# Kernel optimization log

Measured on AMD Instinct MI355X. Metric: run time of the kernel, lower is better.

The kernel has to match this reference:

```python
import jax, jax.numpy as jnp
import numpy as np

B, T, H, N = 4, 2048, 1024, 16
DT_MIN, DT_MAX = 1e-3, 1e-1
A_INIT_MIN, A_INIT_MAX = 0.5, 2.0


def _inv_softplus(x):
    # log(exp(x) - 1), numerically stable
    return x + jnp.log(-jnp.expm1(-x))


def setup_inputs() -> dict:
    key = jax.random.key(0)
    kx, ka, kb, kc, kw, kdt = jax.random.split(key, 6)
    x = jax.random.normal(kx, (B, T, H), dtype=jnp.float32)
    A_log = jax.random.uniform(ka, (H, N), minval=np.log(A_INIT_MIN), maxval=np.log(A_INIT_MAX), dtype=jnp.float32)
    B_mat = 0.02 * jax.random.normal(kb, (H, N), dtype=jnp.float32)
    C_mat = 0.02 * jax.random.normal(kc, (H, N), dtype=jnp.float32)
    D_vec = jnp.ones((H,), dtype=jnp.float32)
    W_dt = 0.02 * jax.random.normal(kw, (H, H), dtype=jnp.float32)
    b_dt = _inv_softplus(jax.random.uniform(kdt, (H,), minval=DT_MIN, maxval=DT_MAX, dtype=jnp.float32))
    return {"x": x, "A_log": A_log, "B_mat": B_mat, "C_mat": C_mat, "D_vec": D_vec, "W_dt": W_dt, "b_dt": b_dt}


def reference(x, A_log, B_mat, C_mat, D_vec, W_dt, b_dt):
    # in_proj is Identity since input_size == hidden_size
    u = x  # (B, T, H)
    A = -jnp.exp(A_log)  # (H, N)
    # dt for all timesteps at once: softplus(u @ W_dt^T + b_dt) -> (B, T, H)
    dt = jax.nn.softplus(jnp.einsum('bth,gh->btg', u, W_dt) + b_dt)
    state0 = jnp.zeros((u.shape[0], A_log.shape[0], A_log.shape[1]), dtype=u.dtype)

    def step(state, inp):
        dt_t, u_t = inp  # (B, H), (B, H)
        dtA = dt_t[..., None]  # (B, H, 1)
        A_bar = jnp.exp(dtA * A)                       # (B, H, N)
        state = A_bar * state + (dtA * B_mat) * u_t[..., None]
        y_t = jnp.einsum('bhn,hn->bh', state, C_mat) + D_vec * u_t
        return state, y_t

    # scan over time axis
    state_final, ys = jax.lax.scan(step, state0, (dt.transpose(1, 0, 2), u.transpose(1, 0, 2)))
    out = ys.transpose(1, 0, 2)  # (B, T, H)
    return out, state_final
```

## Files before the change

kernel.cpp:

```cpp
#include <hip/hip_runtime.h>
#include <stdint.h>

#define BB 4
#define TT 2048
#define HH 1024
#define NN 16
#define KK 1024
#define GG 1024
#define MM (BB*TT)
#define NCHUNK 64
#define TC (TT/NCHUNK)
#define HB 256

#if __has_builtin(__builtin_amdgcn_exp2f)
#define FAST_EXP2(x) __builtin_amdgcn_exp2f(x)
#else
#define FAST_EXP2(x) __expf((x) * 0.6931471805599453f)
#endif
#define EXPSCALE 1.4426950408889634f

typedef __attribute__((ext_vector_type(8))) short short8;
typedef __attribute__((ext_vector_type(4))) float f32x4;
typedef __attribute__((ext_vector_type(8))) _Float16 half8;
typedef __attribute__((ext_vector_type(4))) _Float16 half4;

__device__ __forceinline__ unsigned short f2bf(float f) {
  union { float f; unsigned u; } a; a.f = f;
  unsigned u = a.u;
  u += 0x7fffu + ((u >> 16) & 1u);
  return (unsigned short)(u >> 16);
}

__global__ __launch_bounds__(256) void cvt2_f32_bf16(const float* __restrict__ srcA,
                                                     unsigned short* __restrict__ dstA, int n4a,
                                                     const float* __restrict__ srcB,
                                                     unsigned short* __restrict__ dstB, int n4b) {
  int i = blockIdx.x * blockDim.x + threadIdx.x;
  const float* s; unsigned short* d; int j;
  if (i < n4a) { s = srcA; d = dstA; j = i; }
  else         { s = srcB; d = dstB; j = i - n4a; if (j >= n4b) return; }
  float4 a = ((const float4*)s)[j];
  ushort4 o;
  o.x = f2bf(a.x); o.y = f2bf(a.y); o.z = f2bf(a.z); o.w = f2bf(a.w);
  ((ushort4*)d)[j] = o;
}

__global__ __launch_bounds__(256) void gemm_dt(const unsigned short* __restrict__ xb,
                                               const unsigned short* __restrict__ wb,
                                               const float* __restrict__ b_dt,
                                               _Float16* __restrict__ dtH) {
  __shared__ short lsA[128 * 32];
  __shared__ short lsB[64 * 32];
  const int tid  = threadIdx.x;
  const int w    = tid >> 6;
  const int lane = tid & 63;
  const int m0 = blockIdx.x * 128;
  const int g0 = blockIdx.y * 64;

  const int ea  = w * 1024 + lane * 8;
  const int am0 = ea >> 5,         ak0 = ea & 31;
  const int am1 = (ea + 512) >> 5, ak1 = (ea + 512) & 31;
  const int eb  = w * 512 + lane * 8;
  const int bg0 = eb >> 5,         bk0 = eb & 31;
  const unsigned short* gA0 = xb + (size_t)(m0 + am0) * KK + ak0;
  const unsigned short* gA1 = xb + (size_t)(m0 + am1) * KK + ak1;
  const unsigned short* gB0 = wb + (size_t)(g0 + bg0) * KK + bk0;
  short* lA0 = lsA + w * 1024;
  short* lB0 = lsB + w * 512;

  const int wm   = (w >> 1) * 64;
  const int wg   = (w & 1) * 32;
  const int lrow = lane & 15;
  const int lq   = lane >> 4;

  f32x4 acc[4][2];
  const f32x4 zero = {0.f, 0.f, 0.f, 0.f};
#pragma unroll
  for (int i = 0; i < 4; ++i)
#pragma unroll
    for (int j = 0; j < 2; ++j) acc[i][j] = zero;

  for (int kt = 0; kt < KK / 32; ++kt) {
    const int ko = kt * 32;
    __builtin_amdgcn_global_load_lds((__attribute__((address_space(1))) void*)(gA0 + ko),
                                     (__attribute__((address_space(3))) void*)(lA0), 16, 0, 0);
    __builtin_amdgcn_global_load_lds((__attribute__((address_space(1))) void*)(gA1 + ko),
                                     (__attribute__((address_space(3))) void*)(lA0 + 512), 16, 0, 0);
    __builtin_amdgcn_global_load_lds((__attribute__((address_space(1))) void*)(gB0 + ko),
                                     (__attribute__((address_space(3))) void*)(lB0), 16, 0, 0);
    __syncthreads();

    short8 af[4], bfr[2];
#pragma unroll
    for (int mi = 0; mi < 4; ++mi)
      af[mi] = *(const short8*)&lsA[(wm + mi * 16 + lrow) * 32 + lq * 8];
#pragma unroll
    for (int ni = 0; ni < 2; ++ni)
      bfr[ni] = *(const short8*)&lsB[(wg + ni * 16 + lrow) * 32 + lq * 8];
#pragma unroll
    for (int mi = 0; mi < 4; ++mi)
#pragma unroll
      for (int ni = 0; ni < 2; ++ni)
        acc[mi][ni] = __builtin_amdgcn_mfma_f32_16x16x32_bf16(af[mi], bfr[ni], acc[mi][ni], 0, 0, 0);
    __syncthreads();
  }

  const int b  = m0 >> 11;
  const int tb = (m0 & (TT - 1)) + wm + lq * 4;
#pragma unroll
  for (int mi = 0; mi < 4; ++mi)
#pragma unroll
    for (int ni = 0; ni < 2; ++ni) {
      const int gcol = g0 + wg + ni * 16 + lrow;
      const float bias = b_dt[gcol];
      half4 sp;
#pragma unroll
      for (int r = 0; r < 4; ++r) {
        float z = acc[mi][ni][r] + bias;
        sp[r] = (_Float16)(fmaxf(z, 0.f) + __logf(1.f + __expf(-fabsf(z))));
      }
      *(half4*)&dtH[((size_t)b * HH + gcol) * TT + tb + mi * 16] = sp;
    }
}

__global__ __launch_bounds__(256, 4) void ssm_phase1(const float* __restrict__ x,
                                                     const _Float16* __restrict__ dtH,
                                                     const float* __restrict__ A_log,
                                                     float* __restrict__ sloc,
                                                     float* __restrict__ sdArr) {
  __shared__ float uT[TC][HB];
  const int tid = threadIdx.x;
  const int bid = blockIdx.x;
  const int hb = bid & (HH / HB - 1);
  const int b  = (bid >> 2) & (BB - 1);
  const int c  = bid >> 4;
  const int h  = hb * HB + tid;
  const int w    = tid >> 6;
  const int lane = tid & 63;

  const float* xg = x + (size_t)b * TT * HH + (size_t)c * TC * HH + hb * HB;
#pragma unroll
  for (int i = 0; i < 8; ++i) {
    const int t = i * 4 + w;
    __builtin_amdgcn_global_load_lds(
        (__attribute__((address_space(1))) void*)(xg + (size_t)t * HH + lane * 4),
        (__attribute__((address_space(3))) void*)&uT[t][0], 16, 0, 0);
  }

  const _Float16* dp = dtH + ((size_t)b * HH + h) * TT + c * TC;
  half8 hv[4];
#pragma unroll
  for (int i = 0; i < 4; ++i) hv[i] = ((const half8*)dp)[i];
  f32x4 dd[8];
#pragma unroll
  for (int i = 0; i < 8; ++i)
#pragma unroll
    for (int k = 0; k < 4; ++k) dd[i][k] = (float)hv[i >> 1][(i & 1) * 4 + k];

  float Ae[NN];
#pragma unroll
  for (int n = 0; n < NN; ++n) Ae[n] = -__expf(A_log[h * NN + n]) * EXPSCALE;

  float s[NN];
#pragma unroll
  for (int n = 0; n < NN; ++n) s[n] = 0.f;
  float sd = 0.f;

  __syncthreads();

#pragma unroll
  for (int jt = 0; jt < 8; ++jt) {
#pragma unroll
    for (int k = 0; k < 4; ++k) {
      const int t = jt * 4 + k;
      const float dtv = dd[jt][k];
      const float du  = dtv * uT[t][tid];
      sd += dtv;
#pragma unroll
      for (int n = 0; n < NN; ++n) {
        const float ab = FAST_EXP2(dtv * Ae[n]);
        s[n] = fmaf(ab, s[n], du);
      }
    }
  }

  float* sp = sloc + (((size_t)c * BB + b) * HH + h) * NN;
#pragma unroll
  for (int n = 0; n < NN; n += 4) {
    f32x4 v = {s[n], s[n + 1], s[n + 2], s[n + 3]};
    *(f32x4*)&sp[n] = v;
  }
  sdArr[((size_t)c * BB + b) * HH + h] = sd;
}

__global__ __launch_bounds__(256) void ssm_phase2(float* __restrict__ sloc,
                                                  const float* __restrict__ sdArr,
                                                  const float* __restrict__ A_log,
                                                  const float* __restrict__ Bm_,
                                                  float* __restrict__ stateOut) {
  const int id = blockIdx.x * 256 + threadIdx.x;
  const int hn = id & (HH * NN - 1);
  const int bh = id >> 4;
  const float Ae = -__expf(A_log[hn]) * EXPSCALE;
  float carry = 0.f;
#pragma unroll 4
  for (int ch = 0; ch < NCHUNK; ++ch) {
    const size_t idx = (size_t)ch * (BB * HH * NN) + id;
    const float sl = sloc[idx];
    const float dc = FAST_EXP2(Ae * sdArr[(size_t)ch * (BB * HH) + bh]);
    sloc[idx] = carry;
    carry = fmaf(dc, carry, sl);
  }
  stateOut[id] = Bm_[hn] * carry;
}

__global__ __launch_bounds__(256, 4) void ssm_phase3(const float* __restrict__ x,
                                                     const _Float16* __restrict__ dtH,
                                                     const float* __restrict__ A_log,
                                                     const float* __restrict__ Bm_,
                                                     const float* __restrict__ Cm_,
                                                     const float* __restrict__ Dv_,
                                                     const float* __restrict__ carryBuf,
                                                     float* __restrict__ out) {
  __shared__ float uT[TC][HB];
  const int tid = threadIdx.x;
  const int bid = blockIdx.x;
  const int hb = bid & (HH / HB - 1);
  const int b  = (bid >> 2) & (BB - 1);
  const int c  = bid >> 4;
  const int h  = hb * HB + tid;
  const int w    = tid >> 6;
  const int lane = tid & 63;

  const float* xg = x + (size_t)b * TT * HH + (size_t)c * TC * HH + hb * HB;
#pragma unroll
  for (int i = 0; i < 8; ++i) {
    const int t = i * 4 + w;
    __builtin_amdgcn_global_load_lds(
        (__attribute__((address_space(1))) void*)(xg + (size_t)t * HH + lane * 4),
        (__attribute__((address_space(3))) void*)&uT[t][0], 16, 0, 0);
  }

  const _Float16* dp = dtH + ((size_t)b * HH + h) * TT + c * TC;
  half8 hv[4];
#pragma unroll
  for (int i = 0; i < 4; ++i) hv[i] = ((const half8*)dp)[i];
  f32x4 dd[8];
#pragma unroll
  for (int i = 0; i < 8; ++i)
#pragma unroll
    for (int k = 0; k < 4; ++k) dd[i][k] = (float)hv[i >> 1][(i & 1) * 4 + k];

  float Ae[NN], Cb[NN];
#pragma unroll
  for (int n = 0; n < NN; ++n) {
    Ae[n] = -__expf(A_log[h * NN + n]) * EXPSCALE;
    Cb[n] = Cm_[h * NN + n] * Bm_[h * NN + n];
  }
  const float Dv = Dv_[h];

  float s[NN];
  const float* cp = carryBuf + (((size_t)c * BB + b) * HH + h) * NN;
#pragma unroll
  for (int n = 0; n < NN; n += 4) {
    f32x4 v = *(const f32x4*)&cp[n];
    s[n] = v[0]; s[n + 1] = v[1]; s[n + 2] = v[2]; s[n + 3] = v[3];
  }

  float* yo = out + (size_t)b * TT * HH + (size_t)c * TC * HH + h;

  __syncthreads();

#pragma unroll
  for (int jt = 0; jt < 8; ++jt) {
#pragma unroll
    for (int k = 0; k < 4; ++k) {
      const int t = jt * 4 + k;
      const float dtv = dd[jt][k];
      const float uv  = uT[t][tid];
      const float du  = dtv * uv;
      float y0 = Dv * uv, y1 = 0.f, y2 = 0.f, y3 = 0.f;
#pragma unroll
      for (int n = 0; n < NN; n += 4) {
        float ab;
        ab = FAST_EXP2(dtv * Ae[n]);     s[n]     = fmaf(ab, s[n],     du); y0 = fmaf(Cb[n],     s[n],     y0);
        ab = FAST_EXP2(dtv * Ae[n + 1]); s[n + 1] = fmaf(ab, s[n + 1], du); y1 = fmaf(Cb[n + 1], s[n + 1], y1);
        ab = FAST_EXP2(dtv * Ae[n + 2]); s[n + 2] = fmaf(ab, s[n + 2], du); y2 = fmaf(Cb[n + 2], s[n + 2], y2);
        ab = FAST_EXP2(dtv * Ae[n + 3]); s[n + 3] = fmaf(ab, s[n + 3], du); y3 = fmaf(Cb[n + 3], s[n + 3], y3);
      }
      yo[(size_t)t * HH] = (y0 + y1) + (y2 + y3);
    }
  }
}

extern "C" void kernel_launch(void* const* d_in, const int* in_sizes, int n_in,
                              void* d_out, int out_size, void* d_ws, size_t ws_size,
                              hipStream_t stream) {
  const float* x     = (const float*)d_in[0];
  const float* A_log = (const float*)d_in[1];
  const float* B_mat = (const float*)d_in[2];
  const float* C_mat = (const float*)d_in[3];
  const float* D_vec = (const float*)d_in[4];
  const float* W_dt  = (const float*)d_in[5];
  const float* b_dt  = (const float*)d_in[6];
  float* out = (float*)d_out;

  char* ws = (char*)d_ws;
  unsigned short* xb  = (unsigned short*)(ws);
  unsigned short* wb  = (unsigned short*)(ws + 16777216);
  _Float16*       dtH = (_Float16*)(ws + 18874368);
  float*          sloc  = (float*)(ws);
  float*          sdArr = (float*)(ws + 16777216);
  float* stateOut = out + (size_t)BB * TT * HH;

  const int n4x = MM * KK / 4, n4w = GG * KK / 4;
  cvt2_f32_bf16<<<(n4x + n4w + 255) / 256, 256, 0, stream>>>(x, xb, n4x, W_dt, wb, n4w);
  gemm_dt<<<dim3(MM / 128, GG / 64), 256, 0, stream>>>(xb, wb, b_dt, dtH);

  const int nblk = (HH / HB) * BB * NCHUNK;
  ssm_phase1<<<nblk, 256, 0, stream>>>(x, dtH, A_log, sloc, sdArr);
  ssm_phase2<<<(BB * HH * NN) / 256, 256, 0, stream>>>(sloc, sdArr, A_log, B_mat, stateOut);
  ssm_phase3<<<nblk, 256, 0, stream>>>(x, dtH, A_log, B_mat, C_mat, D_vec, sloc, out);
}
```

Baseline: 187.8 us.

## Store dt in time-major layout and read scan inputs directly from global

The GEMM epilogue now writes dt as (B,T,H) in fp16 instead of (B,H,T), so the scan kernels can read x and dt per timestep with coalesced per-thread global loads. The LDS staging of x and the barrier are removed from both scan phases. The GEMM grid is also flattened with a block-index swizzle to group tiles for better cache reuse. The GEMM epilogue now issues scalar 2-byte stores scattered across rows, which may cost more store bandwidth than the previous half4 stores.

```diff
diff --git a/kernel.cpp b/kernel.cpp
--- a/kernel.cpp
+++ b/kernel.cpp
@@ -21,8 +21,6 @@
 
 typedef __attribute__((ext_vector_type(8))) short short8;
 typedef __attribute__((ext_vector_type(4))) float f32x4;
-typedef __attribute__((ext_vector_type(8))) _Float16 half8;
-typedef __attribute__((ext_vector_type(4))) _Float16 half4;
 
 __device__ __forceinline__ unsigned short f2bf(float f) {
   union { float f; unsigned u; } a; a.f = f;
@@ -54,8 +52,10 @@
   const int tid  = threadIdx.x;
   const int w    = tid >> 6;
   const int lane = tid & 63;
-  const int m0 = blockIdx.x * 128;
-  const int g0 = blockIdx.y * 64;
+  const int bid  = blockIdx.x;
+  const int swz  = (bid & 7) * 128 + (bid >> 3);
+  const int m0 = (swz >> 4) * 128;
+  const int g0 = (swz & 15) * 64;
 
   const int ea  = w * 1024 + lane * 8;
   const int am0 = ea >> 5,         ak0 = ea & 31;
@@ -105,22 +105,20 @@
     __syncthreads();
   }
 
-  const int b  = m0 >> 11;
-  const int tb = (m0 & (TT - 1)) + wm + lq * 4;
-#pragma unroll
-  for (int mi = 0; mi < 4; ++mi)
-#pragma unroll
-    for (int ni = 0; ni < 2; ++ni) {
-      const int gcol = g0 + wg + ni * 16 + lrow;
-      const float bias = b_dt[gcol];
-      half4 sp;
+  const int mrow = m0 + wm + lq * 4;
+#pragma unroll
+  for (int ni = 0; ni < 2; ++ni) {
+    const int g = g0 + wg + ni * 16 + lrow;
+    const float bias = b_dt[g];
+#pragma unroll
+    for (int mi = 0; mi < 4; ++mi)
 #pragma unroll
       for (int r = 0; r < 4; ++r) {
         float z = acc[mi][ni][r] + bias;
-        sp[r] = (_Float16)(fmaxf(z, 0.f) + __logf(1.f + __expf(-fabsf(z))));
+        dtH[(size_t)(mrow + mi * 16 + r) * GG + g] =
+            (_Float16)(fmaxf(z, 0.f) + __logf(1.f + __expf(-fabsf(z))));
       }
-      *(half4*)&dtH[((size_t)b * HH + gcol) * TT + tb + mi * 16] = sp;
-    }
+  }
 }
 
 __global__ __launch_bounds__(256, 4) void ssm_phase1(const float* __restrict__ x,
@@ -128,34 +126,16 @@
                                                      const float* __restrict__ A_log,
                                                      float* __restrict__ sloc,
                                                      float* __restrict__ sdArr) {
-  __shared__ float uT[TC][HB];
   const int tid = threadIdx.x;
   const int bid = blockIdx.x;
   const int hb = bid & (HH / HB - 1);
   const int b  = (bid >> 2) & (BB - 1);
   const int c  = bid >> 4;
   const int h  = hb * HB + tid;
-  const int w    = tid >> 6;
-  const int lane = tid & 63;
-
-  const float* xg = x + (size_t)b * TT * HH + (size_t)c * TC * HH + hb * HB;
-#pragma unroll
-  for (int i = 0; i < 8; ++i) {
-    const int t = i * 4 + w;
-    __builtin_amdgcn_global_load_lds(
-        (__attribute__((address_space(1))) void*)(xg + (size_t)t * HH + lane * 4),
-        (__attribute__((address_space(3))) void*)&uT[t][0], 16, 0, 0);
-  }
-
-  const _Float16* dp = dtH + ((size_t)b * HH + h) * TT + c * TC;
-  half8 hv[4];
-#pragma unroll
-  for (int i = 0; i < 4; ++i) hv[i] = ((const half8*)dp)[i];
-  f32x4 dd[8];
-#pragma unroll
-  for (int i = 0; i < 8; ++i)
-#pragma unroll
-    for (int k = 0; k < 4; ++k) dd[i][k] = (float)hv[i >> 1][(i & 1) * 4 + k];
+
+  const size_t base = ((size_t)b * TT + c * TC) * HH + h;
+  const float*    up = x + base;
+  const _Float16* dp = dtH + base;
 
   float Ae[NN];
 #pragma unroll
@@ -166,15 +146,18 @@
   for (int n = 0; n < NN; ++n) s[n] = 0.f;
   float sd = 0.f;
 
-  __syncthreads();
-
-#pragma unroll
-  for (int jt = 0; jt < 8; ++jt) {
-#pragma unroll
-    for (int k = 0; k < 4; ++k) {
-      const int t = jt * 4 + k;
-      const float dtv = dd[jt][k];
-      const float du  = dtv * uT[t][tid];
+#pragma unroll
+  for (int j = 0; j < TC / 8; ++j) {
+    float uu[8], dv[8];
+#pragma unroll
+    for (int i = 0; i < 8; ++i) {
+      uu[i] = up[(size_t)(j * 8 + i) * HH];
+      dv[i] = (float)dp[(size_t)(j * 8 + i) * HH];
+    }
+#pragma unroll
+    for (int i = 0; i < 8; ++i) {
+      const float dtv = dv[i];
+      const float du  = dtv * uu[i];
       sd += dtv;
 #pragma unroll
       for (int n = 0; n < NN; ++n) {
@@ -222,34 +205,17 @@
                                                      const float* __restrict__ Dv_,
                                                      const float* __restrict__ carryBuf,
                                                      float* __restrict__ out) {
-  __shared__ float uT[TC][HB];
   const int tid = threadIdx.x;
   const int bid = blockIdx.x;
   const int hb = bid & (HH / HB - 1);
   const int b  = (bid >> 2) & (BB - 1);
   const int c  = bid >> 4;
   const int h  = hb * HB + tid;
-  const int w    = tid >> 6;
-  const int lane = tid & 63;
-
-  const float* xg = x + (size_t)b * TT * HH + (size_t)c * TC * HH + hb * HB;
-#pragma unroll
-  for (int i = 0; i < 8; ++i) {
-    const int t = i * 4 + w;
-    __builtin_amdgcn_global_load_lds(
-        (__attribute__((address_space(1))) void*)(xg + (size_t)t * HH + lane * 4),
-        (__attribute__((address_space(3))) void*)&uT[t][0], 16, 0, 0);
-  }
-
-  const _Float16* dp = dtH + ((size_t)b * HH + h) * TT + c * TC;
-  half8 hv[4];
-#pragma unroll
-  for (int i = 0; i < 4; ++i) hv[i] = ((const half8*)dp)[i];
-  f32x4 dd[8];
-#pragma unroll
-  for (int i = 0; i < 8; ++i)
-#pragma unroll
-    for (int k = 0; k < 4; ++k) dd[i][k] = (float)hv[i >> 1][(i & 1) * 4 + k];
+
+  const size_t base = ((size_t)b * TT + c * TC) * HH + h;
+  const float*    up = x + base;
+  const _Float16* dp = dtH + base;
+  float*          yo = out + base;
 
   float Ae[NN], Cb[NN];
 #pragma unroll
@@ -267,17 +233,18 @@
     s[n] = v[0]; s[n + 1] = v[1]; s[n + 2] = v[2]; s[n + 3] = v[3];
   }
 
-  float* yo = out + (size_t)b * TT * HH + (size_t)c * TC * HH + h;
-
-  __syncthreads();
-
-#pragma unroll
-  for (int jt = 0; jt < 8; ++jt) {
-#pragma unroll
-    for (int k = 0; k < 4; ++k) {
-      const int t = jt * 4 + k;
-      const float dtv = dd[jt][k];
-      const float uv  = uT[t][tid];
+#pragma unroll
+  for (int j = 0; j < TC / 8; ++j) {
+    float uu[8], dv[8];
+#pragma unroll
+    for (int i = 0; i < 8; ++i) {
+      uu[i] = up[(size_t)(j * 8 + i) * HH];
+      dv[i] = (float)dp[(size_t)(j * 8 + i) * HH];
+    }
+#pragma unroll
+    for (int i = 0; i < 8; ++i) {
+      const float dtv = dv[i];
+      const float uv  = uu[i];
       const float du  = dtv * uv;
       float y0 = Dv * uv, y1 = 0.f, y2 = 0.f, y3 = 0.f;
 #pragma unroll
@@ -288,7 +255,7 @@
         ab = FAST_EXP2(dtv * Ae[n + 2]); s[n + 2] = fmaf(ab, s[n + 2], du); y2 = fmaf(Cb[n + 2], s[n + 2], y2);
         ab = FAST_EXP2(dtv * Ae[n + 3]); s[n + 3] = fmaf(ab, s[n + 3], du); y3 = fmaf(Cb[n + 3], s[n + 3], y3);
       }
-      yo[(size_t)t * HH] = (y0 + y1) + (y2 + y3);
+      yo[(size_t)(j * 8 + i) * HH] = (y0 + y1) + (y2 + y3);
     }
   }
 }
@@ -315,7 +282,7 @@
 
   const int n4x = MM * KK / 4, n4w = GG * KK / 4;
   cvt2_f32_bf16<<<(n4x + n4w + 255) / 256, 256, 0, stream>>>(x, xb, n4x, W_dt, wb, n4w);
-  gemm_dt<<<dim3(MM / 128, GG / 64), 256, 0, stream>>>(xb, wb, b_dt, dtH);
+  gemm_dt<<<(MM / 128) * (GG / 64), 256, 0, stream>>>(xb, wb, b_dt, dtH);
 
   const int nblk = (HH / HB) * BB * NCHUNK;
   ssm_phase1<<<nblk, 256, 0, stream>>>(x, dtH, A_log, sloc, sdArr);
```

Result: faster. 183.4 us (-2.3%).
